# Optimization experiments

Measured on AMD Instinct MI355X. Metric: run time of the kernel, lower is better.

## Reference

```python
import jax, jax.numpy as jnp
import numpy as np

B, S, D, H = 512, 2048, 19, 40
LN_EPS = 1e-5


def setup_inputs() -> dict:
    key = jax.random.key(0)
    ks = jax.random.split(key, 12)
    s_ih = 1.0 / np.sqrt(D)
    s_hh = 1.0 / np.sqrt(H)
    inp = {
        "x": jax.random.normal(ks[0], (B, S, D), dtype=jnp.float32),
        "W_ih": jax.random.normal(ks[1], (4 * H, D), dtype=jnp.float32) * s_ih,
        "W_hh": jax.random.normal(ks[2], (4 * H, H), dtype=jnp.float32) * s_hh,
        # PyTorch init: biases zero except forget-gate slice set to 1.0
        "b_ih": jnp.zeros((4 * H,), jnp.float32).at[H:2 * H].set(1.0),
        "b_hh": jnp.zeros((4 * H,), jnp.float32),
        "ln_g": jnp.ones((H,), jnp.float32),
        "ln_b": jnp.zeros((H,), jnp.float32),
        "W1": jax.random.normal(ks[3], (H, H), dtype=jnp.float32) * s_hh,
        "b1": jnp.zeros((H,), jnp.float32),
        "W2": jax.random.normal(ks[4], (H, H), dtype=jnp.float32) * s_hh,
        "b2": jnp.zeros((H,), jnp.float32),
        "Wo": jax.random.normal(ks[5], (1, H), dtype=jnp.float32) * s_hh,
        "bo": jnp.zeros((1,), jnp.float32),
        "log_threshold": jnp.asarray(np.log(0.35), dtype=jnp.float32),
    }
    return inp


def reference(x, W_ih, W_hh, b_ih, b_hh, ln_g, ln_b, W1, b1, W2, b2, Wo, bo, log_threshold):
    Bx, Sx, _ = x.shape
    Hh = W_hh.shape[1]
    # Precompute input contribution to all gates: [B, S, 4H]
    xg = jnp.einsum('bsd,gd->bsg', x, W_ih) + (b_ih + b_hh)

    def step(carry, xg_t):
        h, c = carry
        gates = xg_t + h @ W_hh.T            # [B, 4H], torch gate order i,f,g,o
        i, f, g, o = jnp.split(gates, 4, axis=-1)
        c = jax.nn.sigmoid(f) * c + jax.nn.sigmoid(i) * jnp.tanh(g)
        h = jax.nn.sigmoid(o) * jnp.tanh(c)
        return (h, c), h

    h0 = jnp.zeros((Bx, Hh), x.dtype)
    (hN, cN), hs = jax.lax.scan(step, (h0, h0), jnp.swapaxes(xg, 0, 1))
    out = jnp.swapaxes(hs, 0, 1)             # [B, S, H]

    # LayerNorm
    mu = out.mean(-1, keepdims=True)
    var = ((out - mu) ** 2).mean(-1, keepdims=True)
    ln = (out - mu) * jax.lax.rsqrt(var + LN_EPS) * ln_g + ln_b

    # Residual tanh-MLP (dropout is identity in eval mode)
    res = jnp.tanh(ln @ W1.T + b1)
    res = jnp.tanh(res @ W2.T + b2)
    y = jax.nn.sigmoid(ln) + res

    raw_sig = jnp.tanh(y @ Wo.T + bo)        # [B, S, 1]
    thr = jnp.exp(log_threshold)
    mask = (jnp.abs(jax.lax.stop_gradient(raw_sig)) >= thr).astype(raw_sig.dtype)
    sig = raw_sig * jax.lax.stop_gradient(mask)
    return sig, (hN[None], cN[None]), thr
```

## Files before the change

kernel.cpp:

```cpp
#include <hip/hip_runtime.h>
#include <math.h>

#define BB 512
#define SS 2048
#define DD 19
#define HH 40
#define CH 32
#define NCH (SS / CH)
#define RS 41
#define HS 48
#define GT 320

#define QPERM(v, ctrl) __int_as_float(__builtin_amdgcn_mov_dpp(__float_as_int(v), (ctrl), 0xf, 0xf, true))
#define HMIR(v) __int_as_float(__builtin_amdgcn_mov_dpp(__float_as_int(v), 0x141, 0xf, 0xf, true))

__device__ __forceinline__ float gate_act(float a, float mulk) {
    float e = __expf(a * mulk);
    float r = __builtin_amdgcn_rcpf(e + 1.0f);
    return fmaf(-mulk, r, 1.0f);
}
__device__ __forceinline__ float tanh_fast(float x) {
    float e = __expf(2.0f * x);
    float r = __builtin_amdgcn_rcpf(e + 1.0f);
    return fmaf(-2.0f, r, 1.0f);
}
__device__ __forceinline__ float sigm_fast(float x) {
    float e = __expf(x);
    float r = __builtin_amdgcn_rcpf(e + 1.0f);
    return fmaf(-1.0f, r, 1.0f);
}

__global__ __launch_bounds__(GT, 1)
void lstm_seq(const float* __restrict__ x,
              const float* __restrict__ W_ih,
              const float* __restrict__ W_hh,
              const float* __restrict__ b_ih,
              const float* __restrict__ b_hh,
              const float* __restrict__ log_thr,
              float* __restrict__ hist,
              float* __restrict__ out) {
    __shared__ __align__(16) float s_h[2][HS];
    __shared__ __align__(16) float s_x[CH][20];
    __shared__ float s_hist[CH][HS];

    const int tid = threadIdx.x;
    const int b = blockIdx.x;
    if (tid < HS) { s_h[0][tid] = 0.0f; s_h[1][tid] = 0.0f; }
    if (tid < CH) s_x[tid][19] = 0.0f;

    const int u = tid >> 3;
    const int half = (tid >> 2) & 1;
    const int g = tid & 3;
    const int grow = g * HH + u;
    const float mulk = (g == 2) ? 2.0f : 1.0f;

    float whh[20];
    {
        const float4* wr = (const float4*)&W_hh[grow * HH + half * 20];
#pragma unroll
        for (int q = 0; q < 5; ++q) {
            float4 f = wr[q];
            whh[4*q] = f.x; whh[4*q+1] = f.y; whh[4*q+2] = f.z; whh[4*q+3] = f.w;
        }
    }
    float wih[10];
#pragma unroll
    for (int d = 0; d < 10; ++d) {
        int idx = half * 10 + d;
        wih[d] = (idx < DD) ? W_ih[grow * DD + idx] : 0.0f;
    }
    const float bsumv = half ? 0.0f : (b_ih[grow] + b_hh[grow]);

    float cc = 0.0f, hh = 0.0f;

    const int i0 = tid, i1 = tid + GT;
    const int st0 = i0 / DD, d0 = i0 % DD;
    const int st1 = i1 / DD, d1 = i1 % DD;
    const bool has1 = (i1 < CH * DD);
    float xr0, xr1 = 0.f;
    {
        const float* xp = x + (size_t)b * SS * DD;
        xr0 = xp[i0];
        if (has1) xr1 = xp[i1];
    }

    float* hb = hist + (size_t)b * SS * HH;
    __syncthreads();

    for (int ch = 0; ch < NCH; ++ch) {
        s_x[st0][d0] = xr0;
        if (has1) s_x[st1][d1] = xr1;
        if (ch + 1 < NCH) {
            const float* xp = x + ((size_t)b * SS + (size_t)(ch + 1) * CH) * DD;
            xr0 = xp[i0];
            if (has1) xr1 = xp[i1];
        }
        __syncthreads();

        float xpart;
        {
            const float* xs = &s_x[0][half * 10];
            float p0 = bsumv, p1 = 0.f;
#pragma unroll
            for (int d = 0; d < 10; d += 2) {
                p0 = fmaf(wih[d], xs[d], p0);
                p1 = fmaf(wih[d + 1], xs[d + 1], p1);
            }
            xpart = p0 + p1;
        }

        for (int t = 0; t < CH; ++t) {
            float xv[10];
            if (t + 1 < CH) {
                const float* xs = &s_x[t + 1][half * 10];
#pragma unroll
                for (int d = 0; d < 10; ++d) xv[d] = xs[d];
            }
            const float4* h4 = (const float4*)&s_h[t & 1][half * 20];
            float a0 = xpart, a1 = 0.f;
#pragma unroll
            for (int q = 0; q < 5; ++q) {
                float4 f = h4[q];
                a0 = fmaf(f.x, whh[4*q+0], a0);
                a1 = fmaf(f.y, whh[4*q+1], a1);
                a0 = fmaf(f.z, whh[4*q+2], a0);
                a1 = fmaf(f.w, whh[4*q+3], a1);
            }
            float acc = a0 + a1;
            float other = QPERM(HMIR(acc), 0x1B);
            float full = acc + other;
            float av = gate_act(full, mulk);
            float bv = QPERM(av, 0xB1);
            float cv = QPERM(av, 0x4E);
            float dv = QPERM(av, 0x1B);
            if ((tid & 7) == 0) {
                cc = fmaf(bv, cc, av * cv);
                hh = dv * tanh_fast(cc);
                s_h[(t + 1) & 1][u] = hh;
                s_hist[t][u] = hh;
            }
            if (t + 1 < CH) {
                float p0 = bsumv, p1 = 0.f;
#pragma unroll
                for (int d = 0; d < 10; d += 2) {
                    p0 = fmaf(wih[d], xv[d], p0);
                    p1 = fmaf(wih[d + 1], xv[d + 1], p1);
                }
                xpart = p0 + p1;
            }
            __syncthreads();
        }

        {
            const size_t cb = (size_t)ch * CH * HH;
#pragma unroll
            for (int it = 0; it < 4; ++it) {
                int i = tid + it * GT;
                hb[cb + i] = s_hist[i / HH][i % HH];
            }
        }
    }

    if ((tid & 7) == 0) {
        out[(size_t)BB * SS + (size_t)b * HH + u] = hh;
        out[(size_t)BB * SS + (size_t)BB * HH + (size_t)b * HH + u] = cc;
    }
    if (b == 0 && tid == 0) {
        out[(size_t)BB * SS + 2 * (size_t)BB * HH] = expf(log_thr[0]);
    }
}

__global__ __launch_bounds__(256, 2)
void post_mlp(const float* __restrict__ hist,
              const float* __restrict__ ln_g,
              const float* __restrict__ ln_b,
              const float* __restrict__ W1,
              const float* __restrict__ b1,
              const float* __restrict__ W2,
              const float* __restrict__ b2,
              const float* __restrict__ Wo,
              const float* __restrict__ bo,
              const float* __restrict__ log_thr,
              float* __restrict__ out) {
    __shared__ float s_rows[256][HH + 1];
    __shared__ __align__(16) float s_W1[HH * HH];
    __shared__ __align__(16) float s_W2[HH * HH];
    __shared__ float s_lng[HH], s_lnb[HH], s_Wo[HH], s_b1[HH], s_b2[HH];

    const int tid = threadIdx.x;
    const size_t base = (size_t)blockIdx.x * 256 * HH;

    for (int i = tid; i < HH * HH; i += 256) { s_W1[i] = W1[i]; s_W2[i] = W2[i]; }
    if (tid < HH) {
        s_lng[tid] = ln_g[tid]; s_lnb[tid] = ln_b[tid]; s_Wo[tid] = Wo[tid];
        s_b1[tid] = b1[tid]; s_b2[tid] = b2[tid];
    }
    for (int i = tid; i < 256 * HH; i += 256)
        s_rows[i / HH][i % HH] = hist[base + i];
    __syncthreads();

    const float bo0 = bo[0];
    const float thrv = expf(log_thr[0]);

    float hv[HH];
#pragma unroll
    for (int k = 0; k < HH; ++k) hv[k] = s_rows[tid][k];
    float m0 = 0.f, m1 = 0.f, q0 = 0.f, q1 = 0.f;
#pragma unroll
    for (int k = 0; k < HH; k += 2) {
        m0 += hv[k]; m1 += hv[k + 1];
        q0 = fmaf(hv[k], hv[k], q0); q1 = fmaf(hv[k + 1], hv[k + 1], q1);
    }
    float mu = (m0 + m1) * (1.0f / HH);
    float var = (q0 + q1) * (1.0f / HH) - mu * mu;
    float inv = 1.0f / sqrtf(var + 1e-5f);
#pragma unroll
    for (int k = 0; k < HH; ++k)
        hv[k] = fmaf((hv[k] - mu) * inv, s_lng[k], s_lnb[k]);

    float part = 0.f;
#pragma unroll
    for (int k = 0; k < HH; ++k)
        part = fmaf(sigm_fast(hv[k]), s_Wo[k], part);

#pragma unroll 2
    for (int j = 0; j < HH; ++j) {
        const float4* wr = (const float4*)&s_W1[j * HH];
        float a0 = s_b1[j], a1 = 0.f;
#pragma unroll
        for (int q = 0; q < 10; ++q) {
            float4 w4 = wr[q];
            a0 = fmaf(w4.x, hv[4*q+0], a0); a1 = fmaf(w4.y, hv[4*q+1], a1);
            a0 = fmaf(w4.z, hv[4*q+2], a0); a1 = fmaf(w4.w, hv[4*q+3], a1);
        }
        s_rows[tid][j] = tanh_fast(a0 + a1);
    }
    float rr[HH];
#pragma unroll
    for (int k = 0; k < HH; ++k) rr[k] = s_rows[tid][k];
#pragma unroll 2
    for (int j = 0; j < HH; ++j) {
        const float4* wr = (const float4*)&s_W2[j * HH];
        float a0 = s_b2[j], a1 = 0.f;
#pragma unroll
        for (int q = 0; q < 10; ++q) {
            float4 w4 = wr[q];
            a0 = fmaf(w4.x, rr[4*q+0], a0); a1 = fmaf(w4.y, rr[4*q+1], a1);
            a0 = fmaf(w4.z, rr[4*q+2], a0); a1 = fmaf(w4.w, rr[4*q+3], a1);
        }
        float r2 = tanh_fast(a0 + a1);
        part = fmaf(r2, s_Wo[j], part);
    }
    float raw = tanh_fast(part + bo0);
    float sg = (fabsf(raw) >= thrv) ? raw : 0.0f;
    out[(size_t)blockIdx.x * 256 + tid] = sg;
}

__global__ __launch_bounds__(256, 2)
void lstm_fused(const float* __restrict__ x, const float* __restrict__ W_ih,
                const float* __restrict__ W_hh, const float* __restrict__ b_ih,
                const float* __restrict__ b_hh, const float* __restrict__ ln_g,
                const float* __restrict__ ln_b, const float* __restrict__ W1,
                const float* __restrict__ b1, const float* __restrict__ W2,
                const float* __restrict__ b2, const float* __restrict__ Wo,
                const float* __restrict__ bo, const float* __restrict__ log_thr,
                float* __restrict__ out) {
    __shared__ float s_ring[CH][RS];
    __shared__ __align__(16) float s_h[2][HS];
    __shared__ __align__(16) float s_x[CH][20];
    __shared__ __align__(16) float s_W1[HH * HH];
    __shared__ __align__(16) float s_W2[HH * HH];
    __shared__ float s_lng[HH], s_lnb[HH], s_Wo[HH], s_b1[HH], s_b2[HH];
    __shared__ float s_part[256];

    const int tid = threadIdx.x;
    const int b = blockIdx.x;
    for (int i = tid; i < HH * HH; i += 256) { s_W1[i] = W1[i]; s_W2[i] = W2[i]; }
    if (tid < HH) {
        s_lng[tid] = ln_g[tid]; s_lnb[tid] = ln_b[tid]; s_Wo[tid] = Wo[tid];
        s_b1[tid] = b1[tid]; s_b2[tid] = b2[tid];
    }
    if (tid < HS) { s_h[0][tid] = 0.0f; s_h[1][tid] = 0.0f; }
    const float bo0 = bo[0];
    const float thrv = expf(log_thr[0]);
    const bool isGate = tid < 4 * HH;
    const int g = tid & 3, u = tid >> 2;
    const int grow = g * HH + u;
    const float mulk = (g == 2) ? 2.0f : 1.0f;
    float wih[DD], whh[HH], bsum = 0.0f;
    if (isGate) {
#pragma unroll
        for (int d = 0; d < DD; ++d) wih[d] = W_ih[grow * DD + d];
        const float4* wr = (const float4*)&W_hh[grow * HH];
#pragma unroll
        for (int q = 0; q < 10; ++q) {
            float4 f = wr[q];
            whh[4*q] = f.x; whh[4*q+1] = f.y; whh[4*q+2] = f.z; whh[4*q+3] = f.w;
        }
        bsum = b_ih[grow] + b_hh[grow];
    }
    float cc = 0.0f, hh = 0.0f;
    const int i0 = tid, i1 = tid + 256, i2 = tid + 512;
    const int st0 = i0 / DD, d0 = i0 % DD;
    const int st1 = i1 / DD, d1 = i1 % DD;
    const int st2 = i2 / DD, d2 = i2 % DD;
    float xr0 = 0.f, xr1 = 0.f, xr2 = 0.f;
    {
        const float* xp = x + (size_t)b * SS * DD;
        xr0 = xp[i0]; xr1 = xp[i1];
        if (i2 < CH * DD) xr2 = xp[i2];
    }
    __syncthreads();
    for (int ch = 0; ch < NCH; ++ch) {
        s_x[st0][d0] = xr0; s_x[st1][d1] = xr1;
        if (i2 < CH * DD) s_x[st2][d2] = xr2;
        if (ch + 1 < NCH) {
            const float* xp = x + ((size_t)b * SS + (size_t)(ch + 1) * CH) * DD;
            xr0 = xp[i0]; xr1 = xp[i1];
            if (i2 < CH * DD) xr2 = xp[i2];
        }
        __syncthreads();
        for (int t = 0; t < CH; ++t) {
            if (isGate) {
                const float4* h4 = (const float4*)s_h[t & 1];
                const float4* x4 = (const float4*)&s_x[t][0];
                float a0 = bsum, a1 = 0.f, a2 = 0.f, a3 = 0.f;
                float4 xa = x4[0], xb = x4[1], xc = x4[2], xd = x4[3], xe = x4[4];
                a0 = fmaf(xa.x, wih[0], a0);  a1 = fmaf(xa.y, wih[1], a1);
                a2 = fmaf(xa.z, wih[2], a2);  a3 = fmaf(xa.w, wih[3], a3);
                a0 = fmaf(xb.x, wih[4], a0);  a1 = fmaf(xb.y, wih[5], a1);
                a2 = fmaf(xb.z, wih[6], a2);  a3 = fmaf(xb.w, wih[7], a3);
                a0 = fmaf(xc.x, wih[8], a0);  a1 = fmaf(xc.y, wih[9], a1);
                a2 = fmaf(xc.z, wih[10], a2); a3 = fmaf(xc.w, wih[11], a3);
                a0 = fmaf(xd.x, wih[12], a0); a1 = fmaf(xd.y, wih[13], a1);
                a2 = fmaf(xd.z, wih[14], a2); a3 = fmaf(xd.w, wih[15], a3);
                a0 = fmaf(xe.x, wih[16], a0); a1 = fmaf(xe.y, wih[17], a1);
                a2 = fmaf(xe.z, wih[18], a2);
#pragma unroll
                for (int q = 0; q < 10; ++q) {
                    float4 f = h4[q];
                    a0 = fmaf(f.x, whh[4*q+0], a0);
                    a1 = fmaf(f.y, whh[4*q+1], a1);
                    a2 = fmaf(f.z, whh[4*q+2], a2);
                    a3 = fmaf(f.w, whh[4*q+3], a3);
                }
                float acc = (a0 + a1) + (a2 + a3);
                float av = gate_act(acc, mulk);
                float bv = __shfl_xor(av, 1);
                float cv = __shfl_xor(av, 2);
                float dv = __shfl_xor(bv, 2);
                if (g == 0) {
                    cc = fmaf(bv, cc, av * cv);
                    hh = dv * tanh_fast(cc);
                    s_h[(t + 1) & 1][u] = hh;
                    s_ring[t][u] = hh;
                }
            }
            __syncthreads();
        }
        {
            const int st = tid & 31;
            const int q8 = tid >> 5;
            float hv[HH];
#pragma unroll
            for (int k = 0; k < HH; ++k) hv[k] = s_ring[st][k];
            float m0 = 0.f, m1 = 0.f, q0 = 0.f, q1 = 0.f;
#pragma unroll
            for (int k = 0; k < HH; k += 2) {
                m0 += hv[k]; m1 += hv[k + 1];
                q0 = fmaf(hv[k], hv[k], q0); q1 = fmaf(hv[k + 1], hv[k + 1], q1);
            }
            float mu = (m0 + m1) * (1.0f / HH);
            float var = (q0 + q1) * (1.0f / HH) - mu * mu;
            float inv = 1.0f / sqrtf(var + 1e-5f);
#pragma unroll
            for (int k = 0; k < HH; ++k)
                hv[k] = fmaf((hv[k] - mu) * inv, s_lng[k], s_lnb[k]);
            float part = 0.f;
#pragma unroll
            for (int k = 0; k < HH; ++k)
                part = fmaf(sigm_fast(hv[k]), s_Wo[k], part);
            if (q8 != 0) part = 0.f;
            __syncthreads();
            float r1v[5];
#pragma unroll
            for (int jj = 0; jj < 5; ++jj) {
                int j = q8 * 5 + jj;
                const float4* wr = (const float4*)&s_W1[j * HH];
                float a0 = s_b1[j], a1 = 0.f;
#pragma unroll
                for (int q = 0; q < 10; ++q) {
                    float4 w4 = wr[q];
                    a0 = fmaf(w4.x, hv[4*q+0], a0); a1 = fmaf(w4.y, hv[4*q+1], a1);
                    a0 = fmaf(w4.z, hv[4*q+2], a0); a1 = fmaf(w4.w, hv[4*q+3], a1);
                }
                r1v[jj] = tanh_fast(a0 + a1);
                s_ring[st][j] = r1v[jj];
            }
            __syncthreads();
            float rr[HH];
#pragma unroll
            for (int k = 0; k < HH; ++k) rr[k] = s_ring[st][k];
#pragma unroll
            for (int jj = 0; jj < 5; ++jj) {
                int j = q8 * 5 + jj;
                const float4* wr = (const float4*)&s_W2[j * HH];
                float a0 = s_b2[j], a1 = 0.f;
#pragma unroll
                for (int q = 0; q < 10; ++q) {
                    float4 w4 = wr[q];
                    a0 = fmaf(w4.x, rr[4*q+0], a0); a1 = fmaf(w4.y, rr[4*q+1], a1);
                    a0 = fmaf(w4.z, rr[4*q+2], a0); a1 = fmaf(w4.w, rr[4*q+3], a1);
                }
                float r2 = tanh_fast(a0 + a1);
                part = fmaf(r2, s_Wo[j], part);
            }
            s_part[tid] = part;
            __syncthreads();
            if (tid < CH) {
                float tot = bo0;
#pragma unroll
                for (int qq = 0; qq < 8; ++qq) tot += s_part[tid + 32 * qq];
                float raw = tanh_fast(tot);
                float sg = (fabsf(raw) >= thrv) ? raw : 0.0f;
                out[(size_t)b * SS + (size_t)ch * CH + tid] = sg;
            }
        }
    }
    if (isGate && g == 0) {
        out[(size_t)BB * SS + (size_t)b * HH + u] = hh;
        out[(size_t)BB * SS + (size_t)BB * HH + (size_t)b * HH + u] = cc;
    }
    if (b == 0 && tid == 0) {
        out[(size_t)BB * SS + 2 * (size_t)BB * HH] = thrv;
    }
}

extern "C" void kernel_launch(void* const* d_in, const int* in_sizes, int n_in,
                              void* d_out, int out_size, void* d_ws, size_t ws_size,
                              hipStream_t stream) {
    const float* x    = (const float*)d_in[0];
    const float* W_ih = (const float*)d_in[1];
    const float* W_hh = (const float*)d_in[2];
    const float* b_ih = (const float*)d_in[3];
    const float* b_hh = (const float*)d_in[4];
    const float* ln_g = (const float*)d_in[5];
    const float* ln_b = (const float*)d_in[6];
    const float* W1   = (const float*)d_in[7];
    const float* b1   = (const float*)d_in[8];
    const float* W2   = (const float*)d_in[9];
    const float* b2   = (const float*)d_in[10];
    const float* Wo   = (const float*)d_in[11];
    const float* bo   = (const float*)d_in[12];
    const float* lt   = (const float*)d_in[13];
    float* out = (float*)d_out;

    const size_t need = (size_t)BB * SS * HH * sizeof(float);
    if (ws_size >= need) {
        float* hist = (float*)d_ws;
        lstm_seq<<<dim3(BB), dim3(GT), 0, stream>>>(
            x, W_ih, W_hh, b_ih, b_hh, lt, hist, out);
        post_mlp<<<dim3(BB * SS / 256), dim3(256), 0, stream>>>(
            hist, ln_g, ln_b, W1, b1, W2, b2, Wo, bo, lt, out);
    } else {
        lstm_fused<<<dim3(BB), dim3(256), 0, stream>>>(
            x, W_ih, W_hh, b_ih, b_hh, ln_g, ln_b, W1, b1, W2, b2, Wo, bo, lt, out);
    }
}
```

Baseline: 890.5 us.

## Precompute input gate projections in separate kernel and use h ring buffer

```diff
diff --git a/kernel.cpp b/kernel.cpp
--- a/kernel.cpp
+++ b/kernel.cpp
@@ -5,6 +5,7 @@
 #define SS 2048
 #define DD 19
 #define HH 40
+#define G4 160
 #define CH 32
 #define NCH (SS / CH)
 #define RS 41
@@ -30,15 +31,153 @@
     return fmaf(-1.0f, r, 1.0f);
 }
 
+__global__ __launch_bounds__(256)
+void xg_pre(const float* __restrict__ x,
+            const float* __restrict__ W_ih,
+            const float* __restrict__ b_ih,
+            const float* __restrict__ b_hh,
+            float* __restrict__ xg) {
+    __shared__ __align__(16) float s_W[G4][20];
+    __shared__ __align__(16) float s_xr[16][20];
+    __shared__ float s_bias[G4];
+
+    const int tid = threadIdx.x;
+    const int bb = blockIdx.x >> 7;
+    const int tg = blockIdx.x & 127;
+    const int t0 = tg * 16;
+
+    for (int i = tid; i < G4 * DD; i += 256) s_W[i / DD][i % DD] = W_ih[i];
+    if (tid < G4) { s_W[tid][19] = 0.0f; s_bias[tid] = b_ih[tid] + b_hh[tid]; }
+    {
+        const float* xp = x + ((size_t)bb * SS + t0) * DD;
+        for (int i = tid; i < 16 * DD; i += 256) s_xr[i / DD][i % DD] = xp[i];
+        if (tid < 16) s_xr[tid][19] = 0.0f;
+    }
+    __syncthreads();
+
+    float* op = xg + ((size_t)bb * SS + t0) * G4;
+#pragma unroll
+    for (int k = 0; k < 10; ++k) {
+        int o = tid + k * 256;
+        int t = o / G4, r = o - t * G4;
+        const float4* wr = (const float4*)&s_W[r][0];
+        const float4* xr4 = (const float4*)&s_xr[t][0];
+        float a0 = s_bias[r], a1 = 0.f;
+#pragma unroll
+        for (int q = 0; q < 5; ++q) {
+            float4 w = wr[q]; float4 f = xr4[q];
+            a0 = fmaf(w.x, f.x, a0); a1 = fmaf(w.y, f.y, a1);
+            a0 = fmaf(w.z, f.z, a0); a1 = fmaf(w.w, f.w, a1);
+        }
+        op[o] = a0 + a1;
+    }
+}
+
 __global__ __launch_bounds__(GT, 1)
-void lstm_seq(const float* __restrict__ x,
-              const float* __restrict__ W_ih,
+void lstm_seq(const float* __restrict__ xg,
               const float* __restrict__ W_hh,
-              const float* __restrict__ b_ih,
-              const float* __restrict__ b_hh,
               const float* __restrict__ log_thr,
               float* __restrict__ hist,
               float* __restrict__ out) {
+    __shared__ __align__(16) float s_ring[CH + 1][HS];
+
+    const int tid = threadIdx.x;
+    const int b = blockIdx.x;
+
+    const int u = tid >> 3;
+    const int half = (tid >> 2) & 1;
+    const int g = tid & 3;
+    const int grow = g * HH + u;
+    const float mulk = (g == 2) ? 2.0f : 1.0f;
+
+    float whh[20];
+    {
+        const float4* wr = (const float4*)&W_hh[grow * HH + half * 20];
+#pragma unroll
+        for (int q = 0; q < 5; ++q) {
+            float4 f = wr[q];
+            whh[4*q] = f.x; whh[4*q+1] = f.y; whh[4*q+2] = f.z; whh[4*q+3] = f.w;
+        }
+    }
+    float cc = 0.0f, hh = 0.0f;
+    if (tid < HH) s_ring[0][tid] = 0.0f;
+
+    const float* xgb = xg + (size_t)b * SS * G4 + grow;
+    float* hb = hist + (size_t)b * SS * HH;
+    float xgr[CH];
+
+    for (int ch = 0; ch < NCH; ++ch) {
+        if (ch > 0) {
+            const size_t cb = (size_t)(ch - 1) * CH * HH;
+#pragma unroll
+            for (int it = 0; it < 4; ++it) {
+                int i = tid + it * GT;
+                hb[cb + i] = s_ring[1 + i / HH][i % HH];
+            }
+            if (tid < HH) s_ring[0][tid] = s_ring[CH][tid];
+        }
+        if (half == 0) {
+            const float* xp = xgb + (size_t)ch * CH * G4;
+#pragma unroll
+            for (int t = 0; t < CH; ++t) xgr[t] = xp[(size_t)t * G4];
+        }
+        __syncthreads();
+
+#pragma unroll
+        for (int t = 0; t < CH; ++t) {
+            const float4* h4 = (const float4*)&s_ring[t][half * 20];
+            float a0 = (half == 0) ? xgr[t] : 0.0f;
+            float a1 = 0.f;
+#pragma unroll
+            for (int q = 0; q < 5; ++q) {
+                float4 f = h4[q];
+                a0 = fmaf(f.x, whh[4*q+0], a0);
+                a1 = fmaf(f.y, whh[4*q+1], a1);
+                a0 = fmaf(f.z, whh[4*q+2], a0);
+                a1 = fmaf(f.w, whh[4*q+3], a1);
+            }
+            float acc = a0 + a1;
+            float other = QPERM(HMIR(acc), 0x1B);
+            float full = acc + other;
+            float av = gate_act(full, mulk);
+            float bv = QPERM(av, 0xB1);
+            float cv = QPERM(av, 0x4E);
+            float dv = QPERM(av, 0x1B);
+            if ((tid & 7) == 0) {
+                cc = fmaf(bv, cc, av * cv);
+                hh = dv * tanh_fast(cc);
+                s_ring[t + 1][u] = hh;
+            }
+            __syncthreads();
+        }
+    }
+
+    {
+        const size_t cb = (size_t)(NCH - 1) * CH * HH;
+#pragma unroll
+        for (int it = 0; it < 4; ++it) {
+            int i = tid + it * GT;
+            hb[cb + i] = s_ring[1 + i / HH][i % HH];
+        }
+    }
+    if ((tid & 7) == 0) {
+        out[(size_t)BB * SS + (size_t)b * HH + u] = hh;
+        out[(size_t)BB * SS + (size_t)BB * HH + (size_t)b * HH + u] = cc;
+    }
+    if (b == 0 && tid == 0) {
+        out[(size_t)BB * SS + 2 * (size_t)BB * HH] = expf(log_thr[0]);
+    }
+}
+
+__global__ __launch_bounds__(GT, 1)
+void lstm_seq2(const float* __restrict__ x,
+               const float* __restrict__ W_ih,
+               const float* __restrict__ W_hh,
+               const float* __restrict__ b_ih,
+               const float* __restrict__ b_hh,
+               const float* __restrict__ log_thr,
+               float* __restrict__ hist,
+               float* __restrict__ out) {
     __shared__ __align__(16) float s_h[2][HS];
     __shared__ __align__(16) float s_x[CH][20];
     __shared__ float s_hist[CH][HS];
@@ -83,7 +222,6 @@
         xr0 = xp[i0];
         if (has1) xr1 = xp[i1];
     }
-
     float* hb = hist + (size_t)b * SS * HH;
     __syncthreads();
 
@@ -96,7 +234,6 @@
             if (has1) xr1 = xp[i1];
         }
         __syncthreads();
-
         float xpart;
         {
             const float* xs = &s_x[0][half * 10];
@@ -108,7 +245,6 @@
             }
             xpart = p0 + p1;
         }
-
         for (int t = 0; t < CH; ++t) {
             float xv[10];
             if (t + 1 < CH) {
@@ -150,7 +286,6 @@
             }
             __syncthreads();
         }
-
         {
             const size_t cb = (size_t)ch * CH * HH;
 #pragma unroll
@@ -160,7 +295,6 @@
             }
         }
     }
-
     if ((tid & 7) == 0) {
         out[(size_t)BB * SS + (size_t)b * HH + u] = hh;
         out[(size_t)BB * SS + (size_t)BB * HH + (size_t)b * HH + u] = cc;
@@ -455,10 +589,18 @@
     const float* lt   = (const float*)d_in[13];
     float* out = (float*)d_out;
 
-    const size_t need = (size_t)BB * SS * HH * sizeof(float);
-    if (ws_size >= need) {
+    const size_t need_hist = (size_t)BB * SS * HH * sizeof(float);
+    const size_t need_xg   = (size_t)BB * SS * G4 * sizeof(float);
+    if (ws_size >= need_hist + need_xg) {
         float* hist = (float*)d_ws;
-        lstm_seq<<<dim3(BB), dim3(GT), 0, stream>>>(
+        float* xg = (float*)((char*)d_ws + need_hist);
+        xg_pre<<<dim3(BB * (SS / 16)), dim3(256), 0, stream>>>(x, W_ih, b_ih, b_hh, xg);
+        lstm_seq<<<dim3(BB), dim3(GT), 0, stream>>>(xg, W_hh, lt, hist, out);
+        post_mlp<<<dim3(BB * SS / 256), dim3(256), 0, stream>>>(
+            hist, ln_g, ln_b, W1, b1, W2, b2, Wo, bo, lt, out);
+    } else if (ws_size >= need_hist) {
+        float* hist = (float*)d_ws;
+        lstm_seq2<<<dim3(BB), dim3(GT), 0, stream>>>(
             x, W_ih, W_hh, b_ih, b_hh, lt, hist, out);
         post_mlp<<<dim3(BB * SS / 256), dim3(256), 0, stream>>>(
             hist, ln_g, ln_b, W1, b1, W2, b2, Wo, bo, lt, out);
```

Result: no change. 890.6 us (+0.0%).

## Add producer warp computing input projection one chunk ahead of recurrence

Applied to the files above, without the earlier changes.

```diff
diff --git a/kernel.cpp b/kernel.cpp
--- a/kernel.cpp
+++ b/kernel.cpp
@@ -5,11 +5,13 @@
 #define SS 2048
 #define DD 19
 #define HH 40
+#define G4 160
 #define CH 32
 #define NCH (SS / CH)
 #define RS 41
 #define HS 48
 #define GT 320
+#define BLK 384
 
 #define QPERM(v, ctrl) __int_as_float(__builtin_amdgcn_mov_dpp(__float_as_int(v), (ctrl), 0xf, 0xf, true))
 #define HMIR(v) __int_as_float(__builtin_amdgcn_mov_dpp(__float_as_int(v), 0x141, 0xf, 0xf, true))
@@ -30,22 +32,24 @@
     return fmaf(-1.0f, r, 1.0f);
 }
 
-__global__ __launch_bounds__(GT, 1)
-void lstm_seq(const float* __restrict__ x,
-              const float* __restrict__ W_ih,
-              const float* __restrict__ W_hh,
-              const float* __restrict__ b_ih,
-              const float* __restrict__ b_hh,
-              const float* __restrict__ log_thr,
-              float* __restrict__ hist,
-              float* __restrict__ out) {
-    __shared__ __align__(16) float s_h[2][HS];
+__global__ __launch_bounds__(BLK, 1)
+void lstm_seqf(const float* __restrict__ x,
+               const float* __restrict__ W_ih,
+               const float* __restrict__ W_hh,
+               const float* __restrict__ b_ih,
+               const float* __restrict__ b_hh,
+               const float* __restrict__ log_thr,
+               float* __restrict__ hist,
+               float* __restrict__ out) {
+    __shared__ __align__(16) float s_ring[CH + 1][HS];
+    __shared__ float s_xg[2][G4][CH + 1];
     __shared__ __align__(16) float s_x[CH][20];
-    __shared__ float s_hist[CH][HS];
 
     const int tid = threadIdx.x;
     const int b = blockIdx.x;
-    if (tid < HS) { s_h[0][tid] = 0.0f; s_h[1][tid] = 0.0f; }
+    const bool isGate = tid < GT;
+
+    if (tid < HH) s_ring[0][tid] = 0.0f;
     if (tid < CH) s_x[tid][19] = 0.0f;
 
     const int u = tid >> 3;
@@ -55,113 +59,166 @@
     const float mulk = (g == 2) ? 2.0f : 1.0f;
 
     float whh[20];
-    {
+    float cc = 0.0f, hh = 0.0f;
+    const int lane = tid - GT;
+    float wx0[DD], wx1[DD], wx2[DD];
+    float bq0 = 0.f, bq1 = 0.f, bq2 = 0.f;
+    float xreg[10];
+    const size_t xbase = (size_t)b * SS * DD;
+
+    if (isGate) {
         const float4* wr = (const float4*)&W_hh[grow * HH + half * 20];
 #pragma unroll
         for (int q = 0; q < 5; ++q) {
             float4 f = wr[q];
             whh[4*q] = f.x; whh[4*q+1] = f.y; whh[4*q+2] = f.z; whh[4*q+3] = f.w;
         }
-    }
-    float wih[10];
-#pragma unroll
-    for (int d = 0; d < 10; ++d) {
-        int idx = half * 10 + d;
-        wih[d] = (idx < DD) ? W_ih[grow * DD + idx] : 0.0f;
-    }
-    const float bsumv = half ? 0.0f : (b_ih[grow] + b_hh[grow]);
-
-    float cc = 0.0f, hh = 0.0f;
-
-    const int i0 = tid, i1 = tid + GT;
-    const int st0 = i0 / DD, d0 = i0 % DD;
-    const int st1 = i1 / DD, d1 = i1 % DD;
-    const bool has1 = (i1 < CH * DD);
-    float xr0, xr1 = 0.f;
-    {
-        const float* xp = x + (size_t)b * SS * DD;
-        xr0 = xp[i0];
-        if (has1) xr1 = xp[i1];
-    }
-
+    } else {
+        const int r0 = lane, r1 = 64 + lane, r2 = 128 + (lane & 31);
+#pragma unroll
+        for (int d = 0; d < DD; ++d) {
+            wx0[d] = W_ih[r0 * DD + d];
+            wx1[d] = W_ih[r1 * DD + d];
+            wx2[d] = W_ih[r2 * DD + d];
+        }
+        bq0 = b_ih[r0] + b_hh[r0];
+        bq1 = b_ih[r1] + b_hh[r1];
+        bq2 = b_ih[r2] + b_hh[r2];
+
+        const float* xp = x + xbase;
+#pragma unroll
+        for (int q = 0; q < 10; ++q) {
+            int i = lane + 64 * q;
+            if (i < CH * DD) s_x[i / DD][i % DD] = xp[i];
+        }
+        asm volatile("s_waitcnt vmcnt(0) lgkmcnt(0)" ::: "memory");
+#pragma unroll 1
+        for (int t = 0; t < CH; ++t) {
+            const float4* xr4 = (const float4*)&s_x[t][0];
+            float4 xA = xr4[0], xB = xr4[1], xC = xr4[2], xD = xr4[3], xE = xr4[4];
+            float xv[20];
+            xv[0]=xA.x; xv[1]=xA.y; xv[2]=xA.z; xv[3]=xA.w;
+            xv[4]=xB.x; xv[5]=xB.y; xv[6]=xB.z; xv[7]=xB.w;
+            xv[8]=xC.x; xv[9]=xC.y; xv[10]=xC.z; xv[11]=xC.w;
+            xv[12]=xD.x; xv[13]=xD.y; xv[14]=xD.z; xv[15]=xD.w;
+            xv[16]=xE.x; xv[17]=xE.y; xv[18]=xE.z;
+            float d0a = bq0, d0b = 0.f, d1a = bq1, d1b = 0.f, d2a = bq2, d2b = 0.f;
+#pragma unroll
+            for (int d = 0; d < 18; d += 2) {
+                d0a = fmaf(wx0[d], xv[d], d0a); d0b = fmaf(wx0[d+1], xv[d+1], d0b);
+                d1a = fmaf(wx1[d], xv[d], d1a); d1b = fmaf(wx1[d+1], xv[d+1], d1b);
+                d2a = fmaf(wx2[d], xv[d], d2a); d2b = fmaf(wx2[d+1], xv[d+1], d2b);
+            }
+            d0a = fmaf(wx0[18], xv[18], d0a);
+            d1a = fmaf(wx1[18], xv[18], d1a);
+            d2a = fmaf(wx2[18], xv[18], d2a);
+            s_xg[0][r0][t] = d0a + d0b;
+            s_xg[0][r1][t] = d1a + d1b;
+            if (lane < 32) s_xg[0][r2][t] = d2a + d2b;
+        }
+        const float* xp1 = x + xbase + CH * DD;
+#pragma unroll
+        for (int q = 0; q < 10; ++q) {
+            int i = lane + 64 * q;
+            xreg[q] = (i < CH * DD) ? xp1[i] : 0.0f;
+        }
+    }
     float* hb = hist + (size_t)b * SS * HH;
     __syncthreads();
 
     for (int ch = 0; ch < NCH; ++ch) {
-        s_x[st0][d0] = xr0;
-        if (has1) s_x[st1][d1] = xr1;
-        if (ch + 1 < NCH) {
-            const float* xp = x + ((size_t)b * SS + (size_t)(ch + 1) * CH) * DD;
-            xr0 = xp[i0];
-            if (has1) xr1 = xp[i1];
+        if (ch > 0) {
+            const size_t cb = (size_t)(ch - 1) * CH * HH;
+#pragma unroll
+            for (int it = 0; it < 4; ++it) {
+                int i = tid + it * BLK;
+                if (i < CH * HH) hb[cb + i] = s_ring[1 + i / HH][i % HH];
+            }
+            if (tid < HH) s_ring[0][tid] = s_ring[CH][tid];
+        }
+        float p = 0.0f;
+        if (isGate && half == 0) p = s_xg[ch & 1][grow][0];
+        if (!isGate && ch + 1 < NCH) {
+#pragma unroll
+            for (int q = 0; q < 10; ++q) {
+                int i = lane + 64 * q;
+                if (i < CH * DD) s_x[i / DD][i % DD] = xreg[q];
+            }
+            if (ch + 2 < NCH) {
+                const float* xp2 = x + xbase + (size_t)(ch + 2) * CH * DD;
+#pragma unroll
+                for (int q = 0; q < 10; ++q) {
+                    int i = lane + 64 * q;
+                    xreg[q] = (i < CH * DD) ? xp2[i] : 0.0f;
+                }
+            }
+            asm volatile("s_waitcnt lgkmcnt(0)" ::: "memory");
         }
         __syncthreads();
 
-        float xpart;
-        {
-            const float* xs = &s_x[0][half * 10];
-            float p0 = bsumv, p1 = 0.f;
-#pragma unroll
-            for (int d = 0; d < 10; d += 2) {
-                p0 = fmaf(wih[d], xs[d], p0);
-                p1 = fmaf(wih[d + 1], xs[d + 1], p1);
-            }
-            xpart = p0 + p1;
-        }
-
         for (int t = 0; t < CH; ++t) {
-            float xv[10];
-            if (t + 1 < CH) {
-                const float* xs = &s_x[t + 1][half * 10];
-#pragma unroll
-                for (int d = 0; d < 10; ++d) xv[d] = xs[d];
-            }
-            const float4* h4 = (const float4*)&s_h[t & 1][half * 20];
-            float a0 = xpart, a1 = 0.f;
-#pragma unroll
-            for (int q = 0; q < 5; ++q) {
-                float4 f = h4[q];
-                a0 = fmaf(f.x, whh[4*q+0], a0);
-                a1 = fmaf(f.y, whh[4*q+1], a1);
-                a0 = fmaf(f.z, whh[4*q+2], a0);
-                a1 = fmaf(f.w, whh[4*q+3], a1);
-            }
-            float acc = a0 + a1;
-            float other = QPERM(HMIR(acc), 0x1B);
-            float full = acc + other;
-            float av = gate_act(full, mulk);
-            float bv = QPERM(av, 0xB1);
-            float cv = QPERM(av, 0x4E);
-            float dv = QPERM(av, 0x1B);
-            if ((tid & 7) == 0) {
-                cc = fmaf(bv, cc, av * cv);
-                hh = dv * tanh_fast(cc);
-                s_h[(t + 1) & 1][u] = hh;
-                s_hist[t][u] = hh;
-            }
-            if (t + 1 < CH) {
-                float p0 = bsumv, p1 = 0.f;
-#pragma unroll
-                for (int d = 0; d < 10; d += 2) {
-                    p0 = fmaf(wih[d], xv[d], p0);
-                    p1 = fmaf(wih[d + 1], xv[d + 1], p1);
-                }
-                xpart = p0 + p1;
+            if (isGate) {
+                const float4* h4 = (const float4*)&s_ring[t][half * 20];
+                float a0 = p, a1 = 0.f;
+#pragma unroll
+                for (int q = 0; q < 5; ++q) {
+                    float4 f = h4[q];
+                    a0 = fmaf(f.x, whh[4*q+0], a0);
+                    a1 = fmaf(f.y, whh[4*q+1], a1);
+                    a0 = fmaf(f.z, whh[4*q+2], a0);
+                    a1 = fmaf(f.w, whh[4*q+3], a1);
+                }
+                if (half == 0 && t + 1 < CH) p = s_xg[ch & 1][grow][t + 1];
+                else p = 0.0f;
+                float acc = a0 + a1;
+                float other = QPERM(HMIR(acc), 0x1B);
+                float full = acc + other;
+                float av = gate_act(full, mulk);
+                float bv = QPERM(av, 0xB1);
+                float cv = QPERM(av, 0x4E);
+                float dv = QPERM(av, 0x1B);
+                if ((tid & 7) == 0) {
+                    cc = fmaf(bv, cc, av * cv);
+                    hh = dv * tanh_fast(cc);
+                    s_ring[t + 1][u] = hh;
+                }
+            } else if (ch + 1 < NCH) {
+                const float4* xr4 = (const float4*)&s_x[t][0];
+                float4 xA = xr4[0], xB = xr4[1], xC = xr4[2], xD = xr4[3], xE = xr4[4];
+                float xv[20];
+                xv[0]=xA.x; xv[1]=xA.y; xv[2]=xA.z; xv[3]=xA.w;
+                xv[4]=xB.x; xv[5]=xB.y; xv[6]=xB.z; xv[7]=xB.w;
+                xv[8]=xC.x; xv[9]=xC.y; xv[10]=xC.z; xv[11]=xC.w;
+                xv[12]=xD.x; xv[13]=xD.y; xv[14]=xD.z; xv[15]=xD.w;
+                xv[16]=xE.x; xv[17]=xE.y; xv[18]=xE.z;
+                float d0a = bq0, d0b = 0.f, d1a = bq1, d1b = 0.f, d2a = bq2, d2b = 0.f;
+#pragma unroll
+                for (int d = 0; d < 18; d += 2) {
+                    d0a = fmaf(wx0[d], xv[d], d0a); d0b = fmaf(wx0[d+1], xv[d+1], d0b);
+                    d1a = fmaf(wx1[d], xv[d], d1a); d1b = fmaf(wx1[d+1], xv[d+1], d1b);
+                    d2a = fmaf(wx2[d], xv[d], d2a); d2b = fmaf(wx2[d+1], xv[d+1], d2b);
+                }
+                d0a = fmaf(wx0[18], xv[18], d0a);
+                d1a = fmaf(wx1[18], xv[18], d1a);
+                d2a = fmaf(wx2[18], xv[18], d2a);
+                const int nb = (ch + 1) & 1;
+                s_xg[nb][lane][t] = d0a + d0b;
+                s_xg[nb][64 + lane][t] = d1a + d1b;
+                if (lane < 32) s_xg[nb][128 + (lane & 31)][t] = d2a + d2b;
             }
             __syncthreads();
         }
-
-        {
-            const size_t cb = (size_t)ch * CH * HH;
-#pragma unroll
-            for (int it = 0; it < 4; ++it) {
-                int i = tid + it * GT;
-                hb[cb + i] = s_hist[i / HH][i % HH];
-            }
-        }
-    }
-
-    if ((tid & 7) == 0) {
+    }
+
+    {
+        const size_t cb = (size_t)(NCH - 1) * CH * HH;
+#pragma unroll
+        for (int it = 0; it < 4; ++it) {
+            int i = tid + it * BLK;
+            if (i < CH * HH) hb[cb + i] = s_ring[1 + i / HH][i % HH];
+        }
+    }
+    if (isGate && (tid & 7) == 0) {
         out[(size_t)BB * SS + (size_t)b * HH + u] = hh;
         out[(size_t)BB * SS + (size_t)BB * HH + (size_t)b * HH + u] = cc;
     }
@@ -455,10 +512,10 @@
     const float* lt   = (const float*)d_in[13];
     float* out = (float*)d_out;
 
-    const size_t need = (size_t)BB * SS * HH * sizeof(float);
-    if (ws_size >= need) {
+    const size_t need_hist = (size_t)BB * SS * HH * sizeof(float);
+    if (ws_size >= need_hist) {
         float* hist = (float*)d_ws;
-        lstm_seq<<<dim3(BB), dim3(GT), 0, stream>>>(
+        lstm_seqf<<<dim3(BB), dim3(BLK), 0, stream>>>(
             x, W_ih, W_hh, b_ih, b_hh, lt, hist, out);
         post_mlp<<<dim3(BB * SS / 256), dim3(256), 0, stream>>>(
             hist, ln_g, ln_b, W1, b1, W2, b2, Wo, bo, lt, out);
```

Measured after the change: 1.458 ms. +63.7%, slower.
